# Kernel optimization log

Measured on AMD Instinct MI355X. Metric: run time of the kernel, lower is better.

## Reference

```python
import jax, jax.numpy as jnp
import numpy as np

B, T, K_EXT, H, P = 256, 336, 16, 512, 256


def setup_inputs() -> dict:
    key = jax.random.key(0)
    ks = jax.random.split(key, 8)
    sH = 1.0 / np.sqrt(H).astype(np.float32)
    sX = 1.0 / np.sqrt(1 + K_EXT).astype(np.float32)
    return {
        "x_l_seq": jax.random.normal(ks[0], (B, T, 1), jnp.float32),
        "x_ext_seq": jax.random.normal(ks[1], (B, T, K_EXT), jnp.float32),
        # meta transform_block params: x_prime = tanh(h@Wh + [x_l,x_ext]@Wx + b_t)
        "Wh": jax.random.normal(ks[2], (H, P), jnp.float32) * sH,
        "Wx": jax.random.normal(ks[3], (1 + K_EXT, P), jnp.float32) * sX,
        "b_t": jnp.zeros((P,), jnp.float32),
        # GRU params (PyTorch layout: gates ordered r, z, n)
        "W_ih": jax.random.normal(ks[4], (3 * H, P), jnp.float32) * sH,
        "W_hh": jax.random.normal(ks[5], (3 * H, H), jnp.float32) * sH,
        "b_ih": jax.random.normal(ks[6], (3 * H,), jnp.float32) * sH,
        "b_hh": jax.random.normal(ks[7], (3 * H,), jnp.float32) * sH,
    }


def reference(x_l_seq, x_ext_seq, Wh, Wx, b_t, W_ih, W_hh, b_ih, b_hh):
    Bb = x_l_seq.shape[0]
    Hh = W_hh.shape[1]
    # concat load + exogenous features once: [B,T,1+K] -> time-major [T,B,1+K]
    xin_tm = jnp.swapaxes(jnp.concatenate([x_l_seq, x_ext_seq], axis=-1), 0, 1)
    h0 = jnp.zeros((Bb, Hh), x_l_seq.dtype)

    def step(h, xin_t):
        # meta-transform: input to GRU depends on current hidden state
        x_prime = jnp.tanh(h @ Wh + xin_t @ Wx + b_t)  # [B,P]
        gx = x_prime @ W_ih.T + b_ih                    # [B,3H]
        gh = h @ W_hh.T + b_hh                          # [B,3H]
        xr, xz, xn = jnp.split(gx, 3, axis=-1)
        hr, hz, hn = jnp.split(gh, 3, axis=-1)
        r = jax.nn.sigmoid(xr + hr)
        z = jax.nn.sigmoid(xz + hz)
        n = jnp.tanh(xn + r * hn)
        h_new = (1.0 - z) * n + z * h
        return h_new, None

    h_final, _ = jax.lax.scan(step, h0, xin_tm)
    return h_final[None]  # [num_layers=1, B, H]
```

## Files before the change

### kernel.cpp

```cpp
#include <hip/hip_runtime.h>
#include <hip/hip_bf16.h>

#define Bn 256
#define Tn 336
#define KE 16

typedef __attribute__((ext_vector_type(8))) __bf16 bf16x8;
typedef __attribute__((ext_vector_type(4))) float f32x4;
typedef unsigned long long u64t;
typedef unsigned int u32t;

#define MFMA(a, b, c) __builtin_amdgcn_mfma_f32_16x16x32_bf16((a), (b), (c), 0, 0, 0)


__global__ void pack_wh(const float* __restrict__ Wh, __bf16* __restrict__ hi,
                        __bf16* __restrict__ lo) {
    int i = blockIdx.x * 256 + threadIdx.x;
    int k = i >> 8, n = i & 255;
    float v = Wh[i];
    __bf16 h = (__bf16)v;
    hi[n * 512 + k] = h;
    lo[n * 512 + k] = (__bf16)(v - (float)h);
}

__global__ void pack_wx(const float* __restrict__ Wx, __bf16* __restrict__ out) {
    int i = blockIdx.x * 256 + threadIdx.x;
    int n = i >> 5, k = i & 31;
    out[i] = (__bf16)((k < 17) ? Wx[k * 256 + n] : 0.f);
}

__global__ void pack_split(const float* __restrict__ in, __bf16* __restrict__ hi,
                           __bf16* __restrict__ lo, int n) {
    int i = blockIdx.x * 256 + threadIdx.x;
    if (i >= n) return;
    float v = in[i];
    __bf16 h = (__bf16)v;
    hi[i] = h;
    lo[i] = (__bf16)(v - (float)h);
}

__global__ void pack_xin(const float* __restrict__ xl, const float* __restrict__ xe,
                         __bf16* __restrict__ out) {
    int i = blockIdx.x * 256 + threadIdx.x;
    int k = i & 31, b = (i >> 5) & 255, t = i >> 13;
    float v = 0.f;
    if (k == 0) v = xl[b * Tn + t];
    else if (k < 17) v = xe[(b * Tn + t) * KE + (k - 1)];
    out[i] = (__bf16)v;
}


__device__ __forceinline__ bf16x8 ld16_mall(const __bf16* p) {
    union { u64t q[2]; bf16x8 v; } r;
    const u64t* q = (const u64t*)p;
    r.q[0] = __hip_atomic_load(q, __ATOMIC_RELAXED, __HIP_MEMORY_SCOPE_AGENT);
    r.q[1] = __hip_atomic_load(q + 1, __ATOMIC_RELAXED, __HIP_MEMORY_SCOPE_AGENT);
    return r.v;
}

__device__ __forceinline__ void st2_mall(__bf16* p, float f) {
    __bf16 h = (__bf16)f;
    union { __bf16 b; unsigned short u; } c; c.b = h;
    __hip_atomic_store((unsigned short*)p, c.u, __ATOMIC_RELAXED,
                       __HIP_MEMORY_SCOPE_AGENT);
}

#define GBAR(VAL)                                                              \
    do {                                                                       \
        __syncthreads();                                                       \
        if (tid == 0)                                                          \
            __hip_atomic_store(fl + l, (u32t)(VAL), __ATOMIC_RELAXED,          \
                               __HIP_MEMORY_SCOPE_AGENT);                      \
        if (w == 0) {                                                          \
            const u32t* fp = fl + (lane & 31);                                 \
            for (;;) {                                                         \
                u32t v = __hip_atomic_load(fp, __ATOMIC_RELAXED,               \
                                           __HIP_MEMORY_SCOPE_AGENT);          \
                if (__all(v >= (u32t)(VAL))) break;                            \
                __builtin_amdgcn_s_sleep(1);                                   \
            }                                                                  \
        }                                                                      \
        __syncthreads();                                                       \
    } while (0)


__global__ __launch_bounds__(512, 2)
__attribute__((amdgpu_waves_per_eu(2, 2)))
void gru_persist(
    const __bf16* __restrict__ WhT_hi, const __bf16* __restrict__ WhT_lo,
    const __bf16* __restrict__ WxTP,
    const __bf16* __restrict__ Wih_hi, const __bf16* __restrict__ Wih_lo,
    const __bf16* __restrict__ Whh_hi, const __bf16* __restrict__ Whh_lo,
    const __bf16* __restrict__ XinP,
    const float* __restrict__ b_t, const float* __restrict__ b_ih,
    const float* __restrict__ b_hh,
    __bf16* xp, __bf16* hbf,
    u32t* cnt, float* __restrict__ out)
{
    __shared__ __align__(16) char lds[106496];

    const int bid = blockIdx.x;
    const int g = bid & 7, l = bid >> 3;
    const int tid = threadIdx.x;
    const int w = tid >> 6, lane = tid & 63;
    const int lr = lane & 15, ko = (lane >> 4) << 3;

    char* hT = lds;
    char* xT = lds + 32768;
    float* ex = (float*)(lds + 49152);
    char* wB = lds + 57344;

    __bf16* hbf_g = hbf + g * (32 * 512);
    __bf16* xp_g  = xp  + g * (32 * 256);
    u32t* fl = cnt + g * 32;

    const int mw = (w == 6) ? (l & 1) : (w & 1);
    const int gg = (w < 6) ? (w >> 1) : 0;

#pragma unroll
    for (int e = 0; e < 3; ++e) {
        int idx = e * 512 + tid;
        int row = idx >> 5, seg = idx & 31;
        int gate = row >> 4, r = row & 15;
        size_t src = (size_t)(gate * 512 + l * 16 + r) * 256 + seg * 8;
        int dst = (row * 512 + seg * 16) ^ ((row & 7) << 4);
        *(bf16x8*)(wB + dst)         = *(const bf16x8*)(Wih_hi + src);
        *(bf16x8*)(wB + 24576 + dst) = *(const bf16x8*)(Wih_lo + src);
    }

    const __bf16 *srcH, *srcL;
    if (w < 6) {
        size_t j = (size_t)(gg * 512 + l * 16 + lr) * 512 + ko;
        srcH = Whh_hi + j; srcL = Whh_lo + j;
    } else if (w == 6) {
        size_t j = (size_t)((l >> 1) * 16 + lr) * 512 + ko;
        srcH = WhT_hi + j; srcL = WhT_lo + j;
    } else {
        srcH = Whh_hi + ko; srcL = Whh_lo + ko;
    }
    f32x4 wHi[16], wLo[16];
#pragma unroll
    for (int k0 = 0; k0 < 16; ++k0) {
        wHi[k0] = *(const f32x4*)(srcH + k0 * 32);
        wLo[k0] = *(const f32x4*)(srcL + k0 * 32);
    }
    bf16x8 wxf = {};
    float bt_r = 0.f;
    if (w == 6) {
        int c = (l >> 1) * 16 + lr;
        wxf = *(const bf16x8*)(WxTP + (size_t)c * 32 + ko);
        bt_r = b_t[c];
    }

    const int erow = tid >> 4, eunit = tid & 15;
    float bi0, bi1, bi2, bh0, bh1, bh2;
    {
        int u = l * 16 + eunit;
        bi0 = b_ih[u]; bi1 = b_ih[512 + u]; bi2 = b_ih[1024 + u];
        bh0 = b_hh[u]; bh1 = b_hh[512 + u]; bh2 = b_hh[1024 + u];
    }
    float hreg = 0.f;
    const int exi = (erow >> 4) * 1024 + (erow & 15) * 16 + eunit;

    const int arow = mw * 16 + lr;
    const int swz = (arow & 7) << 4;
    const int abaseH = arow * 1024 + (lane >> 4) * 16;
    const int abaseX = arow * 512 + (lane >> 4) * 16;
    const int brow = gg * 16 + lr;
    const int bswz = (brow & 7) << 4;
    const int bbase = brow * 512 + (lane >> 4) * 16;

    for (int t = 0; t < Tn; ++t) {
#pragma unroll
        for (int k0 = 0; k0 < 16; ++k0)
            asm volatile("" : "+v"(wHi[k0]), "+v"(wLo[k0]));

#pragma unroll
        for (int e = 0; e < 4; ++e) {
            int r = e * 8 + w;
            bf16x8 v = ld16_mall(hbf_g + r * 512 + lane * 8);
            *(bf16x8*)(hT + ((r * 1024 + lane * 16) ^ ((r & 7) << 4))) = v;
        }
        __syncthreads();

        f32x4 accG = {};
        if (w < 7) {
            f32x4 aH = {}, aL = {};
#pragma unroll
            for (int k0 = 0; k0 < 16; ++k0) {
                bf16x8 a = *(const bf16x8*)(hT + ((abaseH + k0 * 64) ^ swz));
                aH = MFMA(a, __builtin_bit_cast(bf16x8, wHi[k0]), aH);
                aL = MFMA(a, __builtin_bit_cast(bf16x8, wLo[k0]), aL);
            }
            if (w == 6) {
                bf16x8 ax = *(const bf16x8*)(XinP +
                    ((size_t)t * 256 + g * 32 + mw * 16 + lr) * 32 + ko);
                aH = MFMA(ax, wxf, aH);
            }
            accG = aH + aL;
        }
        if (w == 6) {
            int c = (l >> 1) * 16 + lr;
#pragma unroll
            for (int r = 0; r < 4; ++r) {
                int row = mw * 16 + (lane >> 4) * 4 + r;
                float v = accG[r] + bt_r;
                float e2 = __expf(2.f * v);
                st2_mall(xp_g + row * 256 + c, 1.f - 2.f / (e2 + 1.f));
            }
        }

        GBAR(2 * t + 1);

#pragma unroll
        for (int e = 0; e < 2; ++e) {
            int r = e * 16 + (tid >> 5);
            int kc = tid & 31;
            bf16x8 v = ld16_mall(xp_g + r * 256 + kc * 8);
            *(bf16x8*)(xT + ((r * 512 + kc * 16) ^ ((r & 7) << 4))) = v;
        }
        __syncthreads();

        if (w < 6) {
            f32x4 xH = {}, xL = {};
#pragma unroll
            for (int k0 = 0; k0 < 8; ++k0) {
                bf16x8 a  = *(const bf16x8*)(xT + ((abaseX + k0 * 64) ^ swz));
                bf16x8 bh = *(const bf16x8*)(wB + ((bbase + k0 * 64) ^ bswz));
                bf16x8 bl = *(const bf16x8*)(wB + 24576 +
                                             ((bbase + k0 * 64) ^ bswz));
                xH = MFMA(a, bh, xH);
                xL = MFMA(a, bl, xL);
            }
            f32x4 accX = xH + xL;
            float* exm = ex + mw * 1024;
            if (gg < 2) {
#pragma unroll
                for (int r = 0; r < 4; ++r)
                    exm[gg * 256 + ((lane >> 4) * 4 + r) * 16 + lr] =
                        accG[r] + accX[r];
            } else {
#pragma unroll
                for (int r = 0; r < 4; ++r) {
                    exm[2 * 256 + ((lane >> 4) * 4 + r) * 16 + lr] = accX[r];
                    exm[3 * 256 + ((lane >> 4) * 4 + r) * 16 + lr] = accG[r];
                }
            }
        }
        __syncthreads();

        {
            float pr = ex[exi]       + bi0 + bh0;
            float pz = ex[exi + 256] + bi1 + bh1;
            float xn = ex[exi + 512] + bi2;
            float hn = ex[exi + 768] + bh2;
            float rr = 1.f / (1.f + __expf(-pr));
            float zz = 1.f / (1.f + __expf(-pz));
            float e2 = __expf(2.f * (xn + rr * hn));
            float nn = 1.f - 2.f / (e2 + 1.f);
            hreg = (1.f - zz) * nn + zz * hreg;
            st2_mall(hbf_g + erow * 512 + l * 16 + eunit, hreg);
            if (t == Tn - 1)
                out[(size_t)(g * 32 + erow) * 512 + l * 16 + eunit] = hreg;
        }

        if (t != Tn - 1) GBAR(2 * t + 2);
    }
}


extern "C" void kernel_launch(void* const* d_in, const int* in_sizes, int n_in,
                              void* d_out, int out_size, void* d_ws, size_t ws_size,
                              hipStream_t stream) {
    const float* x_l = (const float*)d_in[0];
    const float* x_e = (const float*)d_in[1];
    const float* Wh  = (const float*)d_in[2];
    const float* Wx  = (const float*)d_in[3];
    const float* bt  = (const float*)d_in[4];
    const float* Wih = (const float*)d_in[5];
    const float* Whh = (const float*)d_in[6];
    const float* bih = (const float*)d_in[7];
    const float* bhh = (const float*)d_in[8];

    char* ws = (char*)d_ws;
    __bf16* WhT_hi = (__bf16*)(ws + 0);
    __bf16* WhT_lo = (__bf16*)(ws + 262144);
    __bf16* WxTP   = (__bf16*)(ws + 524288);
    __bf16* Wih_hi = (__bf16*)(ws + 540672);
    __bf16* Wih_lo = (__bf16*)(ws + 1327104);
    __bf16* Whh_hi = (__bf16*)(ws + 2113536);
    __bf16* Whh_lo = (__bf16*)(ws + 3686400);
    __bf16* XinP   = (__bf16*)(ws + 5259264);
    __bf16* xp     = (__bf16*)(ws + 10764288);
    __bf16* hbf    = (__bf16*)(ws + 10895360);
    u32t*   cnt    = (u32t*)  (ws + 11157504);

    pack_wh<<<512, 256, 0, stream>>>(Wh, WhT_hi, WhT_lo);
    pack_wx<<<32, 256, 0, stream>>>(Wx, WxTP);
    pack_split<<<1536, 256, 0, stream>>>(Wih, Wih_hi, Wih_lo, 1536 * 256);
    pack_split<<<3072, 256, 0, stream>>>(Whh, Whh_hi, Whh_lo, 1536 * 512);
    pack_xin<<<10752, 256, 0, stream>>>(x_l, x_e, XinP);
    hipMemsetAsync(hbf, 0, 262144, stream);
    hipMemsetAsync(cnt, 0, 1024, stream);

    gru_persist<<<256, 512, 0, stream>>>(
        WhT_hi, WhT_lo, WxTP, Wih_hi, Wih_lo, Whh_hi, Whh_lo, XinP,
        bt, bih, bhh, xp, hbf, cnt, (float*)d_out);
}
```

Measured before the change: 1.953 ms.

## Replace group barriers with per-half-batch point-to-point flags and double-buffered hidden state

Replaces the two all-block group barriers per timestep with per-producer flags. The 32-row batch group is split into two 16-row halves that wait only on the blocks producing their data, and the hidden state is double-buffered so a step can read the previous h while other blocks write the next. It also splits the K dimension of the hidden GEMM across wave pairs and stages results in LDS, so stores go out as 16-byte vectors instead of 2-byte scalars. The aim is to shorten critical-path synchronisation and allow overlap between halves, at the cost of more __syncthreads, more flag polling and doubled hidden-state memory.

```diff
diff --git a/kernel.cpp b/kernel.cpp
--- a/kernel.cpp
+++ b/kernel.cpp
@@ -11,6 +11,8 @@
 typedef unsigned int u32t;
 
 #define MFMA(a, b, c) __builtin_amdgcn_mfma_f32_16x16x32_bf16((a), (b), (c), 0, 0, 0)
+#define BC8(x) __builtin_bit_cast(bf16x8, (x))
+#define VDRAIN() asm volatile("s_waitcnt vmcnt(0)" ::: "memory")
 
 
 __global__ void pack_wh(const float* __restrict__ Wh, __bf16* __restrict__ hi,
@@ -50,6 +52,12 @@
 }
 
 
+__device__ __forceinline__ u32t ald32(const u32t* p) {
+    return __hip_atomic_load(p, __ATOMIC_RELAXED, __HIP_MEMORY_SCOPE_AGENT);
+}
+__device__ __forceinline__ void ast32(u32t* p, u32t v) {
+    __hip_atomic_store(p, v, __ATOMIC_RELAXED, __HIP_MEMORY_SCOPE_AGENT);
+}
 __device__ __forceinline__ bf16x8 ld16_mall(const __bf16* p) {
     union { u64t q[2]; bf16x8 v; } r;
     const u64t* q = (const u64t*)p;
@@ -57,31 +65,11 @@
     r.q[1] = __hip_atomic_load(q + 1, __ATOMIC_RELAXED, __HIP_MEMORY_SCOPE_AGENT);
     return r.v;
 }
-
-__device__ __forceinline__ void st2_mall(__bf16* p, float f) {
-    __bf16 h = (__bf16)f;
-    union { __bf16 b; unsigned short u; } c; c.b = h;
-    __hip_atomic_store((unsigned short*)p, c.u, __ATOMIC_RELAXED,
-                       __HIP_MEMORY_SCOPE_AGENT);
-}
-
-#define GBAR(VAL)                                                              \
-    do {                                                                       \
-        __syncthreads();                                                       \
-        if (tid == 0)                                                          \
-            __hip_atomic_store(fl + l, (u32t)(VAL), __ATOMIC_RELAXED,          \
-                               __HIP_MEMORY_SCOPE_AGENT);                      \
-        if (w == 0) {                                                          \
-            const u32t* fp = fl + (lane & 31);                                 \
-            for (;;) {                                                         \
-                u32t v = __hip_atomic_load(fp, __ATOMIC_RELAXED,               \
-                                           __HIP_MEMORY_SCOPE_AGENT);          \
-                if (__all(v >= (u32t)(VAL))) break;                            \
-                __builtin_amdgcn_s_sleep(1);                                   \
-            }                                                                  \
-        }                                                                      \
-        __syncthreads();                                                       \
-    } while (0)
+__device__ __forceinline__ void st16_mall(__bf16* p, f32x4 v) {
+    union { f32x4 f; u64t q[2]; } u; u.f = v;
+    __hip_atomic_store((u64t*)p, u.q[0], __ATOMIC_RELAXED, __HIP_MEMORY_SCOPE_AGENT);
+    __hip_atomic_store((u64t*)p + 1, u.q[1], __ATOMIC_RELAXED, __HIP_MEMORY_SCOPE_AGENT);
+}
 
 
 __global__ __launch_bounds__(512, 2)
@@ -97,25 +85,27 @@
     __bf16* xp, __bf16* hbf,
     u32t* cnt, float* __restrict__ out)
 {
-    __shared__ __align__(16) char lds[106496];
+    __shared__ __align__(16) char lds[92672];
+
+    char* hT = lds;
+    char* xT = lds + 16384;
+    float* exG = (float*)(lds + 24576);
+    float* exX = (float*)(lds + 36864);
+    char* pk = lds + 43008;
+    char* wB = lds + 43520;
 
     const int bid = blockIdx.x;
     const int g = bid & 7, l = bid >> 3;
     const int tid = threadIdx.x;
     const int w = tid >> 6, lane = tid & 63;
     const int lr = lane & 15, ko = (lane >> 4) << 3;
-
-    char* hT = lds;
-    char* xT = lds + 32768;
-    float* ex = (float*)(lds + 49152);
-    char* wB = lds + 57344;
-
-    __bf16* hbf_g = hbf + g * (32 * 512);
-    __bf16* xp_g  = xp  + g * (32 * 256);
-    u32t* fl = cnt + g * 32;
-
-    const int mw = (w == 6) ? (l & 1) : (w & 1);
-    const int gg = (w < 6) ? (w >> 1) : 0;
+    const int gg = w >> 1, kh = w & 1;
+    const int cb = l >> 1, myc = l & 1;
+
+    __bf16* xp_g = xp + g * (2 * 16 * 256);
+    const int HBP = 8 * 32 * 512;
+    __bf16* hb_g = hbf + g * (32 * 512);
+    u32t* fl = cnt + g * 128;
 
 #pragma unroll
     for (int e = 0; e < 3; ++e) {
@@ -128,31 +118,31 @@
         *(bf16x8*)(wB + 24576 + dst) = *(const bf16x8*)(Wih_lo + src);
     }
 
-    const __bf16 *srcH, *srcL;
+    const __bf16 *sH0, *sL0, *sH1, *sL1;
     if (w < 6) {
-        size_t j = (size_t)(gg * 512 + l * 16 + lr) * 512 + ko;
-        srcH = Whh_hi + j; srcL = Whh_lo + j;
-    } else if (w == 6) {
-        size_t j = (size_t)((l >> 1) * 16 + lr) * 512 + ko;
-        srcH = WhT_hi + j; srcL = WhT_lo + j;
+        size_t j = (size_t)(gg * 512 + l * 16 + lr) * 512 + kh * 256 + ko;
+        sH0 = Whh_hi + j; sL0 = Whh_lo + j; sH1 = sH0; sL1 = sL0;
     } else {
-        srcH = Whh_hi + ko; srcL = Whh_lo + ko;
+        size_t j = (size_t)(cb * 16 + lr) * 512 + ko;
+        sH0 = WhT_hi + j; sL0 = WhT_lo + j; sH1 = sH0 + 256; sL1 = sL0 + 256;
     }
     f32x4 wHi[16], wLo[16];
 #pragma unroll
-    for (int k0 = 0; k0 < 16; ++k0) {
-        wHi[k0] = *(const f32x4*)(srcH + k0 * 32);
-        wLo[k0] = *(const f32x4*)(srcL + k0 * 32);
+    for (int k0 = 0; k0 < 8; ++k0) {
+        wHi[k0]     = *(const f32x4*)(sH0 + k0 * 32);
+        wLo[k0]     = *(const f32x4*)(sL0 + k0 * 32);
+        wHi[8 + k0] = *(const f32x4*)(sH1 + k0 * 32);
+        wLo[8 + k0] = *(const f32x4*)(sL1 + k0 * 32);
     }
     bf16x8 wxf = {};
     float bt_r = 0.f;
     if (w == 6) {
-        int c = (l >> 1) * 16 + lr;
-        wxf = *(const bf16x8*)(WxTP + (size_t)c * 32 + ko);
-        bt_r = b_t[c];
+        wxf = *(const bf16x8*)(WxTP + (size_t)(cb * 16 + lr) * 32 + ko);
+        bt_r = b_t[cb * 16 + lr];
     }
 
     const int erow = tid >> 4, eunit = tid & 15;
+    const int ecoh = erow >> 4, er = erow & 15;
     float bi0, bi1, bi2, bh0, bh1, bh2;
     {
         int u = l * 16 + eunit;
@@ -160,111 +150,158 @@
         bh0 = b_hh[u]; bh1 = b_hh[512 + u]; bh2 = b_hh[1024 + u];
     }
     float hreg = 0.f;
-    const int exi = (erow >> 4) * 1024 + (erow & 15) * 16 + eunit;
-
-    const int arow = mw * 16 + lr;
-    const int swz = (arow & 7) << 4;
-    const int abaseH = arow * 1024 + (lane >> 4) * 16;
-    const int abaseX = arow * 512 + (lane >> 4) * 16;
-    const int brow = gg * 16 + lr;
-    const int bswz = (brow & 7) << 4;
-    const int bbase = brow * 512 + (lane >> 4) * 16;
+
+    __syncthreads();
 
     for (int t = 0; t < Tn; ++t) {
+        const int hprev = (t & 1) ^ 1, hcur = t & 1;
+        const u32t tg = (u32t)(t + 1);
+
 #pragma unroll
         for (int k0 = 0; k0 < 16; ++k0)
             asm volatile("" : "+v"(wHi[k0]), "+v"(wLo[k0]));
 
-#pragma unroll
-        for (int e = 0; e < 4; ++e) {
-            int r = e * 8 + w;
-            bf16x8 v = ld16_mall(hbf_g + r * 512 + lane * 8);
-            *(bf16x8*)(hT + ((r * 1024 + lane * 16) ^ ((r & 7) << 4))) = v;
+        for (int c = 0; c < 2; ++c) {
+            if (w == 0) {
+                const u32t* fp = fl + 64 + c * 32 + (lane & 31);
+                for (;;) {
+                    u32t v = ald32(fp);
+                    if (__all((int)(v >= (u32t)t))) break;
+                    __builtin_amdgcn_s_sleep(1);
+                }
+            }
+            __syncthreads();
+            {
+                const __bf16* hsrc = hb_g + hprev * HBP + c * (16 * 512);
+#pragma unroll
+                for (int e = 0; e < 2; ++e) {
+                    int idx = e * 512 + tid;
+                    int row = idx >> 6, seg = idx & 63;
+                    bf16x8 v = ld16_mall(hsrc + row * 512 + seg * 8);
+                    *(bf16x8*)(hT + ((row * 1024 + seg * 16) ^ ((row & 7) << 4))) = v;
+                }
+            }
+            __syncthreads();
+            if (w < 6) {
+                f32x4 aH = {}, aL = {};
+#pragma unroll
+                for (int k0 = 0; k0 < 8; ++k0) {
+                    bf16x8 a = *(const bf16x8*)(hT +
+                        ((lr * 1024 + kh * 512 + (lane >> 4) * 16 + k0 * 64) ^
+                         ((lr & 7) << 4)));
+                    aH = MFMA(a, BC8(wHi[k0]), aH);
+                    aL = MFMA(a, BC8(wLo[k0]), aL);
+                }
+                f32x4 acc = aH + aL;
+                float* dst = exG + ((c * 3 + gg) * 2 + kh) * 256;
+#pragma unroll
+                for (int r = 0; r < 4; ++r)
+                    dst[((lane >> 4) * 4 + r) * 16 + lr] = acc[r];
+            } else if (w == 6 && myc == c) {
+                f32x4 aH = {}, aL = {};
+#pragma unroll
+                for (int q = 0; q < 16; ++q) {
+                    int k6 = q >> 3, k0 = q & 7;
+                    bf16x8 a = *(const bf16x8*)(hT +
+                        ((lr * 1024 + k6 * 512 + (lane >> 4) * 16 + k0 * 64) ^
+                         ((lr & 7) << 4)));
+                    aH = MFMA(a, BC8(wHi[q]), aH);
+                    aL = MFMA(a, BC8(wLo[q]), aL);
+                }
+                bf16x8 ax = *(const bf16x8*)(XinP +
+                    ((size_t)t * 256 + g * 32 + c * 16 + lr) * 32 + ko);
+                aH = MFMA(ax, wxf, aH);
+                f32x4 acc = aH + aL;
+#pragma unroll
+                for (int r = 0; r < 4; ++r) {
+                    int row = (lane >> 4) * 4 + r;
+                    float e2 = __expf(2.f * (acc[r] + bt_r));
+                    float tv = 1.f - 2.f / (e2 + 1.f);
+                    *(__bf16*)(pk + (row * 16 + lr) * 2) = (__bf16)tv;
+                }
+                if (lane < 32) {
+                    f32x4 pv = *(const f32x4*)(pk + lane * 16);
+                    st16_mall(xp_g + c * 4096 + (lane >> 1) * 256 + cb * 16 +
+                              (lane & 1) * 8, pv);
+                }
+                VDRAIN();
+                if (lane == 0) ast32(fl + c * 32 + cb, tg);
+            }
         }
-        __syncthreads();
-
-        f32x4 accG = {};
-        if (w < 7) {
-            f32x4 aH = {}, aL = {};
-#pragma unroll
-            for (int k0 = 0; k0 < 16; ++k0) {
-                bf16x8 a = *(const bf16x8*)(hT + ((abaseH + k0 * 64) ^ swz));
-                aH = MFMA(a, __builtin_bit_cast(bf16x8, wHi[k0]), aH);
-                aL = MFMA(a, __builtin_bit_cast(bf16x8, wLo[k0]), aL);
-            }
-            if (w == 6) {
-                bf16x8 ax = *(const bf16x8*)(XinP +
-                    ((size_t)t * 256 + g * 32 + mw * 16 + lr) * 32 + ko);
-                aH = MFMA(ax, wxf, aH);
-            }
-            accG = aH + aL;
+
+        for (int c = 0; c < 2; ++c) {
+            if (w == 0) {
+                const u32t* fp = fl + c * 32 + (lane & 15);
+                for (;;) {
+                    u32t v = ald32(fp);
+                    if (__all((int)(v >= tg))) break;
+                    __builtin_amdgcn_s_sleep(1);
+                }
+            }
+            __syncthreads();
+            {
+                int row = tid >> 5, seg = tid & 31;
+                bf16x8 v = ld16_mall(xp_g + c * 4096 + row * 256 + seg * 8);
+                *(bf16x8*)(xT + ((row * 512 + seg * 16) ^ ((row & 7) << 4))) = v;
+            }
+            __syncthreads();
+            if (w < 6) {
+                f32x4 xH = {}, xL = {};
+                int brow = gg * 16 + lr;
+                int bsw = (brow & 7) << 4;
+                int bb = brow * 512 + (lane >> 4) * 16;
+#pragma unroll
+                for (int k0 = 0; k0 < 4; ++k0) {
+                    int kk = kh * 4 + k0;
+                    bf16x8 a = *(const bf16x8*)(xT +
+                        ((lr * 512 + (lane >> 4) * 16 + kk * 64) ^ ((lr & 7) << 4)));
+                    bf16x8 bh = *(const bf16x8*)(wB + ((bb + kk * 64) ^ bsw));
+                    bf16x8 bl = *(const bf16x8*)(wB + 24576 + ((bb + kk * 64) ^ bsw));
+                    xH = MFMA(a, bh, xH);
+                    xL = MFMA(a, bl, xL);
+                }
+                f32x4 acc = xH + xL;
+                float* dst = exX + (gg * 2 + kh) * 256;
+#pragma unroll
+                for (int r = 0; r < 4; ++r)
+                    dst[((lane >> 4) * 4 + r) * 16 + lr] = acc[r];
+            }
+            __syncthreads();
+            if (ecoh == c) {
+                int i = er * 16 + eunit;
+                float ghr = exG[((c * 3 + 0) * 2) * 256 + i] +
+                            exG[((c * 3 + 0) * 2 + 1) * 256 + i];
+                float ghz = exG[((c * 3 + 1) * 2) * 256 + i] +
+                            exG[((c * 3 + 1) * 2 + 1) * 256 + i];
+                float ghn = exG[((c * 3 + 2) * 2) * 256 + i] +
+                            exG[((c * 3 + 2) * 2 + 1) * 256 + i];
+                float gxr = exX[0 * 256 + i] + exX[1 * 256 + i];
+                float gxz = exX[2 * 256 + i] + exX[3 * 256 + i];
+                float gxn = exX[4 * 256 + i] + exX[5 * 256 + i];
+                float pr = gxr + ghr + bi0 + bh0;
+                float pz = gxz + ghz + bi1 + bh1;
+                float xn = gxn + bi2;
+                float hn = ghn + bh2;
+                float rr = 1.f / (1.f + __expf(-pr));
+                float zz = 1.f / (1.f + __expf(-pz));
+                float e2 = __expf(2.f * (xn + rr * hn));
+                float nn = 1.f - 2.f / (e2 + 1.f);
+                hreg = (1.f - zz) * nn + zz * hreg;
+                *(__bf16*)(pk + i * 2) = (__bf16)hreg;
+                if (t == Tn - 1)
+                    out[(size_t)(g * 32 + erow) * 512 + l * 16 + eunit] = hreg;
+            }
+            __syncthreads();
+            if (w == 0) {
+                if (lane < 32) {
+                    f32x4 pv = *(const f32x4*)(pk + lane * 16);
+                    st16_mall(hb_g + hcur * HBP + (c * 16 + (lane >> 1)) * 512 +
+                              l * 16 + (lane & 1) * 8, pv);
+                }
+                VDRAIN();
+                if (lane == 0) ast32(fl + 64 + c * 32 + l, tg);
+            }
         }
-        if (w == 6) {
-            int c = (l >> 1) * 16 + lr;
-#pragma unroll
-            for (int r = 0; r < 4; ++r) {
-                int row = mw * 16 + (lane >> 4) * 4 + r;
-                float v = accG[r] + bt_r;
-                float e2 = __expf(2.f * v);
-                st2_mall(xp_g + row * 256 + c, 1.f - 2.f / (e2 + 1.f));
-            }
-        }
-
-        GBAR(2 * t + 1);
-
-#pragma unroll
-        for (int e = 0; e < 2; ++e) {
-            int r = e * 16 + (tid >> 5);
-            int kc = tid & 31;
-            bf16x8 v = ld16_mall(xp_g + r * 256 + kc * 8);
-            *(bf16x8*)(xT + ((r * 512 + kc * 16) ^ ((r & 7) << 4))) = v;
-        }
-        __syncthreads();
-
-        if (w < 6) {
-            f32x4 xH = {}, xL = {};
-#pragma unroll
-            for (int k0 = 0; k0 < 8; ++k0) {
-                bf16x8 a  = *(const bf16x8*)(xT + ((abaseX + k0 * 64) ^ swz));
-                bf16x8 bh = *(const bf16x8*)(wB + ((bbase + k0 * 64) ^ bswz));
-                bf16x8 bl = *(const bf16x8*)(wB + 24576 +
-                                             ((bbase + k0 * 64) ^ bswz));
-                xH = MFMA(a, bh, xH);
-                xL = MFMA(a, bl, xL);
-            }
-            f32x4 accX = xH + xL;
-            float* exm = ex + mw * 1024;
-            if (gg < 2) {
-#pragma unroll
-                for (int r = 0; r < 4; ++r)
-                    exm[gg * 256 + ((lane >> 4) * 4 + r) * 16 + lr] =
-                        accG[r] + accX[r];
-            } else {
-#pragma unroll
-                for (int r = 0; r < 4; ++r) {
-                    exm[2 * 256 + ((lane >> 4) * 4 + r) * 16 + lr] = accX[r];
-                    exm[3 * 256 + ((lane >> 4) * 4 + r) * 16 + lr] = accG[r];
-                }
-            }
-        }
-        __syncthreads();
-
-        {
-            float pr = ex[exi]       + bi0 + bh0;
-            float pz = ex[exi + 256] + bi1 + bh1;
-            float xn = ex[exi + 512] + bi2;
-            float hn = ex[exi + 768] + bh2;
-            float rr = 1.f / (1.f + __expf(-pr));
-            float zz = 1.f / (1.f + __expf(-pz));
-            float e2 = __expf(2.f * (xn + rr * hn));
-            float nn = 1.f - 2.f / (e2 + 1.f);
-            hreg = (1.f - zz) * nn + zz * hreg;
-            st2_mall(hbf_g + erow * 512 + l * 16 + eunit, hreg);
-            if (t == Tn - 1)
-                out[(size_t)(g * 32 + erow) * 512 + l * 16 + eunit] = hreg;
-        }
-
-        if (t != Tn - 1) GBAR(2 * t + 2);
     }
 }
 
@@ -293,15 +330,15 @@
     __bf16* XinP   = (__bf16*)(ws + 5259264);
     __bf16* xp     = (__bf16*)(ws + 10764288);
     __bf16* hbf    = (__bf16*)(ws + 10895360);
-    u32t*   cnt    = (u32t*)  (ws + 11157504);
+    u32t*   cnt    = (u32t*)  (ws + 11419648);
 
     pack_wh<<<512, 256, 0, stream>>>(Wh, WhT_hi, WhT_lo);
     pack_wx<<<32, 256, 0, stream>>>(Wx, WxTP);
     pack_split<<<1536, 256, 0, stream>>>(Wih, Wih_hi, Wih_lo, 1536 * 256);
     pack_split<<<3072, 256, 0, stream>>>(Whh, Whh_hi, Whh_lo, 1536 * 512);
     pack_xin<<<10752, 256, 0, stream>>>(x_l, x_e, XinP);
-    hipMemsetAsync(hbf, 0, 262144, stream);
-    hipMemsetAsync(cnt, 0, 1024, stream);
+    hipMemsetAsync(hbf, 0, 524288, stream);
+    hipMemsetAsync(cnt, 0, 4096, stream);
 
     gru_persist<<<256, 512, 0, stream>>>(
         WhT_hi, WhT_lo, WxTP, Wih_hi, Wih_lo, Whh_hi, Whh_lo, XinP,
```

Result: slower. 2.183 ms (+11.8%).

## Replace block-wide grid barriers with producer-only flags and packed 16-byte stores

Applied to the files above, without the earlier changes.

Replaces the two full-group barriers per timestep with split flag arrays. Only wave 6 publishes the x_prime tile and sets a flag after draining its stores. Wave 7 waits, so the other waves no longer spin together, and the hidden-state wait moves to the start of the next step. Per-element 2-byte atomic stores of x_prime and h are packed through LDS into 16-byte stores, which cuts store transactions. The XinP load is hoisted ahead of the wait. The correctness of the memory ordering now depends on the vmcnt drain before each flag store.

```diff
diff --git a/kernel.cpp b/kernel.cpp
--- a/kernel.cpp
+++ b/kernel.cpp
@@ -11,6 +11,8 @@
 typedef unsigned int u32t;
 
 #define MFMA(a, b, c) __builtin_amdgcn_mfma_f32_16x16x32_bf16((a), (b), (c), 0, 0, 0)
+#define BC8(x) __builtin_bit_cast(bf16x8, (x))
+#define VDRAIN() asm volatile("s_waitcnt vmcnt(0)" ::: "memory")
 
 
 __global__ void pack_wh(const float* __restrict__ Wh, __bf16* __restrict__ hi,
@@ -50,6 +52,12 @@
 }
 
 
+__device__ __forceinline__ u32t ald32(const u32t* p) {
+    return __hip_atomic_load(p, __ATOMIC_RELAXED, __HIP_MEMORY_SCOPE_AGENT);
+}
+__device__ __forceinline__ void ast32(u32t* p, u32t v) {
+    __hip_atomic_store(p, v, __ATOMIC_RELAXED, __HIP_MEMORY_SCOPE_AGENT);
+}
 __device__ __forceinline__ bf16x8 ld16_mall(const __bf16* p) {
     union { u64t q[2]; bf16x8 v; } r;
     const u64t* q = (const u64t*)p;
@@ -57,31 +65,11 @@
     r.q[1] = __hip_atomic_load(q + 1, __ATOMIC_RELAXED, __HIP_MEMORY_SCOPE_AGENT);
     return r.v;
 }
-
-__device__ __forceinline__ void st2_mall(__bf16* p, float f) {
-    __bf16 h = (__bf16)f;
-    union { __bf16 b; unsigned short u; } c; c.b = h;
-    __hip_atomic_store((unsigned short*)p, c.u, __ATOMIC_RELAXED,
-                       __HIP_MEMORY_SCOPE_AGENT);
-}
-
-#define GBAR(VAL)                                                              \
-    do {                                                                       \
-        __syncthreads();                                                       \
-        if (tid == 0)                                                          \
-            __hip_atomic_store(fl + l, (u32t)(VAL), __ATOMIC_RELAXED,          \
-                               __HIP_MEMORY_SCOPE_AGENT);                      \
-        if (w == 0) {                                                          \
-            const u32t* fp = fl + (lane & 31);                                 \
-            for (;;) {                                                         \
-                u32t v = __hip_atomic_load(fp, __ATOMIC_RELAXED,               \
-                                           __HIP_MEMORY_SCOPE_AGENT);          \
-                if (__all(v >= (u32t)(VAL))) break;                            \
-                __builtin_amdgcn_s_sleep(1);                                   \
-            }                                                                  \
-        }                                                                      \
-        __syncthreads();                                                       \
-    } while (0)
+__device__ __forceinline__ void st16_mall(__bf16* p, f32x4 v) {
+    union { f32x4 f; u64t q[2]; } u; u.f = v;
+    __hip_atomic_store((u64t*)p, u.q[0], __ATOMIC_RELAXED, __HIP_MEMORY_SCOPE_AGENT);
+    __hip_atomic_store((u64t*)p + 1, u.q[1], __ATOMIC_RELAXED, __HIP_MEMORY_SCOPE_AGENT);
+}
 
 
 __global__ __launch_bounds__(512, 2)
@@ -97,7 +85,14 @@
     __bf16* xp, __bf16* hbf,
     u32t* cnt, float* __restrict__ out)
 {
-    __shared__ __align__(16) char lds[106496];
+    __shared__ __align__(16) char lds[108032];
+
+    char* hT = lds;
+    char* xT = lds + 32768;
+    float* ex = (float*)(lds + 49152);
+    char* pkX = lds + 57344;
+    char* pkH = lds + 57856;
+    char* wB = lds + 58880;
 
     const int bid = blockIdx.x;
     const int g = bid & 7, l = bid >> 3;
@@ -105,17 +100,13 @@
     const int w = tid >> 6, lane = tid & 63;
     const int lr = lane & 15, ko = (lane >> 4) << 3;
 
-    char* hT = lds;
-    char* xT = lds + 32768;
-    float* ex = (float*)(lds + 49152);
-    char* wB = lds + 57344;
-
-    __bf16* hbf_g = hbf + g * (32 * 512);
-    __bf16* xp_g  = xp  + g * (32 * 256);
-    u32t* fl = cnt + g * 32;
+    __bf16* hb_g = hbf + g * (32 * 512);
+    __bf16* xp_g = xp + g * (32 * 256);
+    u32t* fl = cnt + g * 128;
 
     const int mw = (w == 6) ? (l & 1) : (w & 1);
     const int gg = (w < 6) ? (w >> 1) : 0;
+    const int cb = l >> 1;
 
 #pragma unroll
     for (int e = 0; e < 3; ++e) {
@@ -133,7 +124,7 @@
         size_t j = (size_t)(gg * 512 + l * 16 + lr) * 512 + ko;
         srcH = Whh_hi + j; srcL = Whh_lo + j;
     } else if (w == 6) {
-        size_t j = (size_t)((l >> 1) * 16 + lr) * 512 + ko;
+        size_t j = (size_t)(cb * 16 + lr) * 512 + ko;
         srcH = WhT_hi + j; srcL = WhT_lo + j;
     } else {
         srcH = Whh_hi + ko; srcL = Whh_lo + ko;
@@ -147,9 +138,8 @@
     bf16x8 wxf = {};
     float bt_r = 0.f;
     if (w == 6) {
-        int c = (l >> 1) * 16 + lr;
-        wxf = *(const bf16x8*)(WxTP + (size_t)c * 32 + ko);
-        bt_r = b_t[c];
+        wxf = *(const bf16x8*)(WxTP + (size_t)(cb * 16 + lr) * 32 + ko);
+        bt_r = b_t[cb * 16 + lr];
     }
 
     const int erow = tid >> 4, eunit = tid & 15;
@@ -170,54 +160,89 @@
     const int bswz = (brow & 7) << 4;
     const int bbase = brow * 512 + (lane >> 4) * 16;
 
+    __syncthreads();
+
     for (int t = 0; t < Tn; ++t) {
+        const u32t tg = (u32t)(t + 1);
+
 #pragma unroll
         for (int k0 = 0; k0 < 16; ++k0)
             asm volatile("" : "+v"(wHi[k0]), "+v"(wLo[k0]));
 
+        bf16x8 ax = {};
+        if (w == 6)
+            ax = *(const bf16x8*)(XinP +
+                ((size_t)t * 256 + g * 32 + mw * 16 + lr) * 32 + ko);
+
+        if (w == 7) {
+            const u32t* fp = fl + 64 + (lane & 31);
+            for (;;) {
+                u32t v = ald32(fp);
+                if (__all((int)(v >= (u32t)t))) break;
+                __builtin_amdgcn_s_sleep(1);
+            }
+        }
+        __syncthreads();
+
 #pragma unroll
         for (int e = 0; e < 4; ++e) {
-            int r = e * 8 + w;
-            bf16x8 v = ld16_mall(hbf_g + r * 512 + lane * 8);
-            *(bf16x8*)(hT + ((r * 1024 + lane * 16) ^ ((r & 7) << 4))) = v;
+            int idx = e * 512 + tid;
+            int row = idx >> 6, seg = idx & 63;
+            bf16x8 v = ld16_mall(hb_g + row * 512 + seg * 8);
+            *(bf16x8*)(hT + ((row * 1024 + seg * 16) ^ ((row & 7) << 4))) = v;
         }
         __syncthreads();
 
         f32x4 accG = {};
-        if (w < 7) {
+        if (w < 6) {
             f32x4 aH = {}, aL = {};
 #pragma unroll
             for (int k0 = 0; k0 < 16; ++k0) {
                 bf16x8 a = *(const bf16x8*)(hT + ((abaseH + k0 * 64) ^ swz));
-                aH = MFMA(a, __builtin_bit_cast(bf16x8, wHi[k0]), aH);
-                aL = MFMA(a, __builtin_bit_cast(bf16x8, wLo[k0]), aL);
-            }
-            if (w == 6) {
-                bf16x8 ax = *(const bf16x8*)(XinP +
-                    ((size_t)t * 256 + g * 32 + mw * 16 + lr) * 32 + ko);
-                aH = MFMA(ax, wxf, aH);
+                aH = MFMA(a, BC8(wHi[k0]), aH);
+                aL = MFMA(a, BC8(wLo[k0]), aL);
             }
             accG = aH + aL;
-        }
-        if (w == 6) {
-            int c = (l >> 1) * 16 + lr;
+        } else if (w == 6) {
+            f32x4 aH = {}, aL = {};
+#pragma unroll
+            for (int k0 = 0; k0 < 16; ++k0) {
+                bf16x8 a = *(const bf16x8*)(hT + ((abaseH + k0 * 64) ^ swz));
+                aH = MFMA(a, BC8(wHi[k0]), aH);
+                aL = MFMA(a, BC8(wLo[k0]), aL);
+            }
+            aH = MFMA(ax, wxf, aH);
+            f32x4 acc = aH + aL;
 #pragma unroll
             for (int r = 0; r < 4; ++r) {
-                int row = mw * 16 + (lane >> 4) * 4 + r;
-                float v = accG[r] + bt_r;
-                float e2 = __expf(2.f * v);
-                st2_mall(xp_g + row * 256 + c, 1.f - 2.f / (e2 + 1.f));
-            }
-        }
-
-        GBAR(2 * t + 1);
+                int row = (lane >> 4) * 4 + r;
+                float e2 = __expf(2.f * (acc[r] + bt_r));
+                float tv = 1.f - 2.f / (e2 + 1.f);
+                *(__bf16*)(pkX + (row * 16 + lr) * 2) = (__bf16)tv;
+            }
+            if (lane < 32) {
+                f32x4 pv = *(const f32x4*)(pkX + lane * 16);
+                st16_mall(xp_g + (mw * 16 + (lane >> 1)) * 256 + cb * 16 +
+                          (lane & 1) * 8, pv);
+            }
+            VDRAIN();
+            if (lane == 0) ast32(fl + l, tg);
+        } else {
+            const u32t* fp = fl + (lane & 31);
+            for (;;) {
+                u32t v = ald32(fp);
+                if (__all((int)(v >= tg))) break;
+                __builtin_amdgcn_s_sleep(1);
+            }
+        }
+        __syncthreads();
 
 #pragma unroll
         for (int e = 0; e < 2; ++e) {
-            int r = e * 16 + (tid >> 5);
-            int kc = tid & 31;
-            bf16x8 v = ld16_mall(xp_g + r * 256 + kc * 8);
-            *(bf16x8*)(xT + ((r * 512 + kc * 16) ^ ((r & 7) << 4))) = v;
+            int idx = e * 512 + tid;
+            int row = idx >> 5, seg = idx & 31;
+            bf16x8 v = ld16_mall(xp_g + row * 256 + seg * 8);
+            *(bf16x8*)(xT + ((row * 512 + seg * 16) ^ ((row & 7) << 4))) = v;
         }
         __syncthreads();
 
@@ -259,12 +284,18 @@
             float e2 = __expf(2.f * (xn + rr * hn));
             float nn = 1.f - 2.f / (e2 + 1.f);
             hreg = (1.f - zz) * nn + zz * hreg;
-            st2_mall(hbf_g + erow * 512 + l * 16 + eunit, hreg);
+            *(__bf16*)(pkH + (erow * 16 + eunit) * 2) = (__bf16)hreg;
             if (t == Tn - 1)
                 out[(size_t)(g * 32 + erow) * 512 + l * 16 + eunit] = hreg;
         }
-
-        if (t != Tn - 1) GBAR(2 * t + 2);
+        __syncthreads();
+
+        if (w == 7) {
+            f32x4 pv = *(const f32x4*)(pkH + lane * 16);
+            st16_mall(hb_g + (lane >> 1) * 512 + l * 16 + (lane & 1) * 8, pv);
+            VDRAIN();
+            if (lane == 0) ast32(fl + 64 + l, tg);
+        }
     }
 }
 
@@ -301,7 +332,7 @@
     pack_split<<<3072, 256, 0, stream>>>(Whh, Whh_hi, Whh_lo, 1536 * 512);
     pack_xin<<<10752, 256, 0, stream>>>(x_l, x_e, XinP);
     hipMemsetAsync(hbf, 0, 262144, stream);
-    hipMemsetAsync(cnt, 0, 1024, stream);
+    hipMemsetAsync(cnt, 0, 4096, stream);
 
     gru_persist<<<256, 512, 0, stream>>>(
         WhT_hi, WhT_lo, WxTP, Wih_hi, Wih_lo, Whh_hi, Whh_lo, XinP,
```

Measured after the change: 2.146 ms. 9.9% more time.
